# Kernel optimization log

Measured on AMD Instinct MI355X. Metric: run time of the kernel, lower is better.

The kernel has to match this reference:

```python
import jax, jax.numpy as jnp
import numpy as np

H = 32  # hidden size


def _lstm_layer(x_sbi, w_ih, w_hh, b_ih, b_hh):
    # x_sbi: [S, B, in]; w_ih: [4H, in]; w_hh: [4H, H] (torch gate order i,f,g,o)
    S, B, _ = x_sbi.shape
    # precompute input projections for all timesteps: [S, B, 4H]
    xg = jnp.einsum('sbi,gi->sbg', x_sbi, w_ih) + (b_ih + b_hh)

    def step(carry, xg_t):
        h, c = carry
        gates = xg_t + h @ w_hh.T  # [B, 4H]
        i, f, g, o = jnp.split(gates, 4, axis=-1)
        i = jax.nn.sigmoid(i)
        f = jax.nn.sigmoid(f)
        g = jnp.tanh(g)
        o = jax.nn.sigmoid(o)
        c = f * c + i * g
        h = o * jnp.tanh(c)
        return (h, c), h

    h0 = jnp.zeros((B, H), x_sbi.dtype)
    c0 = jnp.zeros((B, H), x_sbi.dtype)
    (h_last, _), hs = jax.lax.scan(step, (h0, c0), xg)
    return hs, h_last  # hs: [S, B, H]


def setup_inputs() -> dict:
    key = jax.random.key(0)
    ks = jax.random.split(key, 12)
    B, S = 4096, 512
    s = 1.0 / np.sqrt(H)  # torch default uniform(-1/sqrt(H), 1/sqrt(H))
    u = lambda k, shape: jax.random.uniform(k, shape, jnp.float32, -s, s)
    return {
        'x': jax.random.normal(ks[0], (B, S, 1), jnp.float32),
        'w_ih0': u(ks[1], (4 * H, 1)),
        'w_hh0': u(ks[2], (4 * H, H)),
        'b_ih0': u(ks[3], (4 * H,)),
        'b_hh0': u(ks[4], (4 * H,)),
        'w_ih1': u(ks[5], (4 * H, H)),
        'w_hh1': u(ks[6], (4 * H, H)),
        'b_ih1': u(ks[7], (4 * H,)),
        'b_hh1': u(ks[8], (4 * H,)),
        'fc1_w': u(ks[9], (16, H)),
        'fc1_b': u(ks[9], (16,)),
        'fc2_w': u(ks[10], (1, 16)),
        'fc2_b': u(ks[11], (1,)),
    }


def reference(x, w_ih0, w_hh0, b_ih0, b_hh0, w_ih1, w_hh1, b_ih1, b_hh1,
              fc1_w, fc1_b, fc2_w, fc2_b):
    x_sbi = jnp.swapaxes(x, 0, 1)  # [S, B, 1]
    hs1, _ = _lstm_layer(x_sbi, w_ih0, w_hh0, b_ih0, b_hh0)
    _, h_last = _lstm_layer(hs1, w_ih1, w_hh1, b_ih1, b_hh1)  # last timestep of layer 2
    y = h_last @ fc1_w.T + fc1_b
    y = jnp.where(y >= 0, y, 0.2 * y)  # leaky_relu(0.2)
    y = y @ fc2_w.T + fc2_b
    return y  # [B, 1]
```

## Files before the change

kernel.cpp:

```cpp
#include <hip/hip_runtime.h>

#define H 32
#define SEQ 512
#define BM 16
#define NTHREADS 512
#define HSTRIDE 40

typedef _Float16 half8 __attribute__((ext_vector_type(8)));
typedef __attribute__((ext_vector_type(4))) float f32x4;

#define L2E 1.44269504088896340736f

__device__ __forceinline__ float rcp_(float x)  { return __builtin_amdgcn_rcpf(x); }
__device__ __forceinline__ float exp2_(float x) { return __builtin_amdgcn_exp2f(x); }
#define MFMA16(A, B, C) __builtin_amdgcn_mfma_f32_16x16x32_f16((A), (B), (C), 0, 0, 0)

__device__ __forceinline__ float cell(const f32x4& g, float& cst) {
    float ei = exp2_(g[0]), ef = exp2_(g[1]), eg = exp2_(g[2]), eo = exp2_(g[3]);
    float A  = 1.f + ei, F = 1.f + ef;
    float Gp = eg + 1.f, Gm = eg - 1.f;
    float t1 = A * Gp;
    float num = fmaf(cst, t1, Gm * F);
    float cn  = num * rcp_(F * t1);
    cst = cn;
    float ec = exp2_(fminf(cn * (2.f * L2E), 80.f));
    return (ec - 1.f) * rcp_((1.f + eo) * (ec + 1.f));
}

__global__ __launch_bounds__(NTHREADS, 2) void lstm_kernel(
    const float* __restrict__ x,
    const float* __restrict__ w_ih0,
    const float* __restrict__ w_hh0,
    const float* __restrict__ b_ih0, const float* __restrict__ b_hh0,
    const float* __restrict__ w_ih1,
    const float* __restrict__ w_hh1,
    const float* __restrict__ b_ih1, const float* __restrict__ b_hh1,
    const float* __restrict__ fc1_w,
    const float* __restrict__ fc1_b,
    const float* __restrict__ fc2_w,
    const float* __restrict__ fc2_b,
    float* __restrict__ out)
{
    __shared__ __align__(16) float    xbufT[SEQ * BM];
    __shared__ __align__(16) _Float16 h1s[4][BM * HSTRIDE];
    __shared__ __align__(16) _Float16 h2s[2][BM * HSTRIDE];
    __shared__ __align__(16) float    h2f[BM * 33];
    __shared__ __align__(16) float    yb[BM * 17];

    const int tid  = threadIdx.x;
    const int lane = tid & 63;
    const int wv   = tid >> 6;
    const int role = wv >> 2;
    const int w    = wv & 3;
    const int c    = lane & 15;
    const int q    = lane >> 4;
    const int r0   = blockIdx.x * BM;

    {
        const int row = tid >> 5;
        const int s0  = (tid & 31) * 16;
        const float* xr = x + (size_t)(r0 + row) * SEQ + s0;
        #pragma unroll
        for (int i = 0; i < 16; i += 4) {
            float4 v = *(const float4*)&xr[i];
            xbufT[(s0 + i + 0) * BM + row] = v.x;
            xbufT[(s0 + i + 1) * BM + row] = v.y;
            xbufT[(s0 + i + 2) * BM + row] = v.z;
            xbufT[(s0 + i + 3) * BM + row] = v.w;
        }
    }
    for (int i = tid; i < 4 * BM * HSTRIDE; i += NTHREADS) ((_Float16*)h1s)[i] = (_Float16)0.f;
    for (int i = tid; i < 2 * BM * HSTRIDE; i += NTHREADS) ((_Float16*)h2s)[i] = (_Float16)0.f;

    const float gsc[4] = { -L2E, -L2E, 2.f * L2E, -L2E };
    const float wsc = gsc[c & 3];
    const int kb = 8 * q;
    const int m = c;

    half8 wA[2], wB[2];
    f32x4 biasv[2], wxv[2];
    int   wof[2];
    #pragma unroll
    for (int k = 0; k < 2; ++k) {
        const int u0    = 8 * w + 4 * k;
        const int u     = u0 + q;
        const int worig = (c & 3) * H + u0 + (c >> 2);
        wof[k] = m * HSTRIDE + u;
        if (role == 0) {
            const float* p = &w_hh0[worig * H + kb];
            #pragma unroll
            for (int j = 0; j < 8; ++j) wA[k][j] = (_Float16)(p[j] * wsc);
            #pragma unroll
            for (int g = 0; g < 4; ++g) {
                biasv[k][g] = (b_ih0[g * H + u] + b_hh0[g * H + u]) * gsc[g];
                wxv[k][g]   = w_ih0[g * H + u] * gsc[g];
            }
        } else {
            const float* p = &w_ih1[worig * H + kb];
            #pragma unroll
            for (int j = 0; j < 8; ++j) wA[k][j] = (_Float16)(p[j] * wsc);
            p = &w_hh1[worig * H + kb];
            #pragma unroll
            for (int j = 0; j < 8; ++j) wB[k][j] = (_Float16)(p[j] * wsc);
            #pragma unroll
            for (int g = 0; g < 4; ++g)
                biasv[k][g] = (b_ih1[g * H + u] + b_hh1[g * H + u]) * gsc[g];
        }
    }

    float cst[2] = {0.f, 0.f};
    float hl[2]  = {0.f, 0.f};

    const int fofs = c * HSTRIDE + kb;

    __syncthreads();

    if (role == 0) __builtin_amdgcn_s_setprio(1);

    float xv = xbufT[m];

    for (int tb = 0; tb < 516; tb += 4) {
        #pragma unroll
        for (int p = 0; p < 4; ++p) {
            const int t = tb + p;
            if (role == 0) {
                if (t < 512) {
                    f32x4 pre[2];
                    #pragma unroll
                    for (int k = 0; k < 2; ++k) {
                        #pragma unroll
                        for (int j = 0; j < 4; ++j) pre[k][j] = fmaf(xv, wxv[k][j], biasv[k][j]);
                    }
                    half8 a1 = *(const half8*)(&h1s[(p + 3) & 3][0] + fofs);
                    f32x4 g1[2];
                    #pragma unroll
                    for (int k = 0; k < 2; ++k) g1[k] = MFMA16(wA[k], a1, pre[k]);
                    #pragma unroll
                    for (int k = 0; k < 2; ++k) {
                        float hv = cell(g1[k], cst[k]);
                        h1s[p][wof[k]] = (_Float16)hv;
                    }
                    int tn = t + 1 < 511 ? t + 1 : 511;
                    xv = xbufT[tn * BM + m];
                }
            } else {
                if (t >= 2 && t < 514) {
                    half8 a1L = *(const half8*)(&h1s[(p + 2) & 3][0] + fofs);
                    half8 a2  = *(const half8*)(&h2s[(p + 1) & 1][0] + fofs);
                    f32x4 g2[2];
                    #pragma unroll
                    for (int k = 0; k < 2; ++k) g2[k] = MFMA16(wB[k], a2, MFMA16(wA[k], a1L, biasv[k]));
                    #pragma unroll
                    for (int k = 0; k < 2; ++k) {
                        float hv = cell(g2[k], cst[k]);
                        hl[k] = hv;
                        h2s[p & 1][wof[k]] = (_Float16)hv;
                    }
                }
            }
            __syncthreads();
        }
    }

    if (role == 0) __builtin_amdgcn_s_setprio(0);

    if (role == 1) {
        #pragma unroll
        for (int k = 0; k < 2; ++k) h2f[m * 33 + (8 * w + 4 * k + q)] = hl[k];
    }
    __syncthreads();
    if (tid < BM * 16) {
        int rr = tid >> 4, j = tid & 15;
        float acc = fc1_b[j];
        #pragma unroll
        for (int k = 0; k < H; ++k) acc += fc1_w[j * H + k] * h2f[rr * 33 + k];
        acc = acc >= 0.f ? acc : 0.2f * acc;
        yb[rr * 17 + j] = acc * fc2_w[j];
    }
    __syncthreads();
    if (tid < BM) {
        float acc = fc2_b[0];
        #pragma unroll
        for (int j = 0; j < 16; ++j) acc += yb[tid * 17 + j];
        out[r0 + tid] = acc;
    }
}

extern "C" void kernel_launch(void* const* d_in, const int* in_sizes, int n_in,
                              void* d_out, int out_size, void* d_ws, size_t ws_size,
                              hipStream_t stream) {
    const float* x     = (const float*)d_in[0];
    const float* w_ih0 = (const float*)d_in[1];
    const float* w_hh0 = (const float*)d_in[2];
    const float* b_ih0 = (const float*)d_in[3];
    const float* b_hh0 = (const float*)d_in[4];
    const float* w_ih1 = (const float*)d_in[5];
    const float* w_hh1 = (const float*)d_in[6];
    const float* b_ih1 = (const float*)d_in[7];
    const float* b_hh1 = (const float*)d_in[8];
    const float* fc1_w = (const float*)d_in[9];
    const float* fc1_b = (const float*)d_in[10];
    const float* fc2_w = (const float*)d_in[11];
    const float* fc2_b = (const float*)d_in[12];
    float* out = (float*)d_out;

    const int B = in_sizes[0] / SEQ;
    hipLaunchKernelGGL(lstm_kernel, dim3(B / BM), dim3(NTHREADS), 0, stream,
                       x, w_ih0, w_hh0, b_ih0, b_hh0, w_ih1, w_hh1, b_ih1, b_hh1,
                       fc1_w, fc1_b, fc2_w, fc2_b, out);
}
```

Before: 264.1 us.

## Precompute layer-2 input projection one step ahead and pack cell math as pairs

Layer-2 waves now compute the W_ih1·h1 MFMA for the next timestep right after their current step, so only the W_hh1 MFMA sits on the recurrent critical path. Hidden-unit assignment is remapped so each lane owns two adjacent units. This allows packed f32x2 cell math and a single 32-bit f16x2 store to LDS. The x buffer gains one padding row so the clamp on the next-x index can be dropped. The cost is extra registers for the double-buffered partial gates, which could hurt occupancy at the 2-blocks launch bound.

```diff
diff --git a/kernel.cpp b/kernel.cpp
--- a/kernel.cpp
+++ b/kernel.cpp
@@ -7,7 +7,9 @@
 #define HSTRIDE 40
 
 typedef _Float16 half8 __attribute__((ext_vector_type(8)));
+typedef _Float16 f16x2 __attribute__((ext_vector_type(2)));
 typedef __attribute__((ext_vector_type(4))) float f32x4;
+typedef __attribute__((ext_vector_type(2))) float f32x2;
 
 #define L2E 1.44269504088896340736f
 
@@ -15,16 +17,24 @@
 __device__ __forceinline__ float exp2_(float x) { return __builtin_amdgcn_exp2f(x); }
 #define MFMA16(A, B, C) __builtin_amdgcn_mfma_f32_16x16x32_f16((A), (B), (C), 0, 0, 0)
 
-__device__ __forceinline__ float cell(const f32x4& g, float& cst) {
-    float ei = exp2_(g[0]), ef = exp2_(g[1]), eg = exp2_(g[2]), eo = exp2_(g[3]);
-    float A  = 1.f + ei, F = 1.f + ef;
-    float Gp = eg + 1.f, Gm = eg - 1.f;
-    float t1 = A * Gp;
-    float num = fmaf(cst, t1, Gm * F);
-    float cn  = num * rcp_(F * t1);
+__device__ __forceinline__ f32x2 cell2(const f32x4& ga, const f32x4& gb, f32x2& cst) {
+    f32x2 ei = {exp2_(ga[0]), exp2_(gb[0])};
+    f32x2 ef = {exp2_(ga[1]), exp2_(gb[1])};
+    f32x2 eg = {exp2_(ga[2]), exp2_(gb[2])};
+    f32x2 eo = {exp2_(ga[3]), exp2_(gb[3])};
+    f32x2 A  = 1.f + ei, F = 1.f + ef;
+    f32x2 Gp = eg + 1.f, Gm = eg - 1.f;
+    f32x2 t1 = A * Gp;
+    f32x2 num = __builtin_elementwise_fma(cst, t1, Gm * F);
+    f32x2 den = F * t1;
+    f32x2 r1 = {rcp_(den.x), rcp_(den.y)};
+    f32x2 cn = num * r1;
     cst = cn;
-    float ec = exp2_(fminf(cn * (2.f * L2E), 80.f));
-    return (ec - 1.f) * rcp_((1.f + eo) * (ec + 1.f));
+    f32x2 arg = __builtin_elementwise_min(cn * (2.f * L2E), (f32x2)80.f);
+    f32x2 ec = {exp2_(arg.x), exp2_(arg.y)};
+    f32x2 dh = (1.f + eo) * (ec + 1.f);
+    f32x2 r2 = {rcp_(dh.x), rcp_(dh.y)};
+    return (ec - 1.f) * r2;
 }
 
 __global__ __launch_bounds__(NTHREADS, 2) void lstm_kernel(
@@ -41,7 +51,7 @@
     const float* __restrict__ fc2_b,
     float* __restrict__ out)
 {
-    __shared__ __align__(16) float    xbufT[SEQ * BM];
+    __shared__ __align__(16) float    xbufT[(SEQ + 1) * BM];
     __shared__ __align__(16) _Float16 h1s[4][BM * HSTRIDE];
     __shared__ __align__(16) _Float16 h2s[2][BM * HSTRIDE];
     __shared__ __align__(16) float    h2f[BM * 33];
@@ -79,13 +89,10 @@
 
     half8 wA[2], wB[2];
     f32x4 biasv[2], wxv[2];
-    int   wof[2];
     #pragma unroll
     for (int k = 0; k < 2; ++k) {
-        const int u0    = 8 * w + 4 * k;
-        const int u     = u0 + q;
-        const int worig = (c & 3) * H + u0 + (c >> 2);
-        wof[k] = m * HSTRIDE + u;
+        const int u     = 8 * w + 2 * q + k;
+        const int worig = (c & 3) * H + 8 * w + 2 * (c >> 2) + k;
         if (role == 0) {
             const float* p = &w_hh0[worig * H + kb];
             #pragma unroll
@@ -108,10 +115,13 @@
         }
     }
 
-    float cst[2] = {0.f, 0.f};
-    float hl[2]  = {0.f, 0.f};
-
-    const int fofs = c * HSTRIDE + kb;
+    f32x2 cst = {0.f, 0.f};
+    f32x2 hl  = {0.f, 0.f};
+
+    const int fofs  = c * HSTRIDE + kb;
+    const int whofs = m * HSTRIDE + 8 * w + 2 * q;
+
+    f32x4 P[2][2] = {};
 
     __syncthreads();
 
@@ -132,30 +142,27 @@
                         for (int j = 0; j < 4; ++j) pre[k][j] = fmaf(xv, wxv[k][j], biasv[k][j]);
                     }
                     half8 a1 = *(const half8*)(&h1s[(p + 3) & 3][0] + fofs);
-                    f32x4 g1[2];
-                    #pragma unroll
-                    for (int k = 0; k < 2; ++k) g1[k] = MFMA16(wA[k], a1, pre[k]);
-                    #pragma unroll
-                    for (int k = 0; k < 2; ++k) {
-                        float hv = cell(g1[k], cst[k]);
-                        h1s[p][wof[k]] = (_Float16)hv;
-                    }
-                    int tn = t + 1 < 511 ? t + 1 : 511;
-                    xv = xbufT[tn * BM + m];
+                    f32x4 g0 = MFMA16(wA[0], a1, pre[0]);
+                    f32x4 g1 = MFMA16(wA[1], a1, pre[1]);
+                    f32x2 hv = cell2(g0, g1, cst);
+                    f16x2 hp; hp[0] = (_Float16)hv.x; hp[1] = (_Float16)hv.y;
+                    *(f16x2*)(&h1s[p][0] + whofs) = hp;
+                    xv = xbufT[(t + 1) * BM + m];
                 }
             } else {
                 if (t >= 2 && t < 514) {
-                    half8 a1L = *(const half8*)(&h1s[(p + 2) & 3][0] + fofs);
-                    half8 a2  = *(const half8*)(&h2s[(p + 1) & 1][0] + fofs);
-                    f32x4 g2[2];
-                    #pragma unroll
-                    for (int k = 0; k < 2; ++k) g2[k] = MFMA16(wB[k], a2, MFMA16(wA[k], a1L, biasv[k]));
-                    #pragma unroll
-                    for (int k = 0; k < 2; ++k) {
-                        float hv = cell(g2[k], cst[k]);
-                        hl[k] = hv;
-                        h2s[p & 1][wof[k]] = (_Float16)hv;
-                    }
+                    half8 a2 = *(const half8*)(&h2s[(p + 1) & 1][0] + fofs);
+                    f32x4 g0 = MFMA16(wB[0], a2, P[p & 1][0]);
+                    f32x4 g1 = MFMA16(wB[1], a2, P[p & 1][1]);
+                    f32x2 hv = cell2(g0, g1, cst);
+                    hl = hv;
+                    f16x2 hp; hp[0] = (_Float16)hv.x; hp[1] = (_Float16)hv.y;
+                    *(f16x2*)(&h2s[p & 1][0] + whofs) = hp;
+                }
+                if (t >= 1 && t < 513) {
+                    half8 a1n = *(const half8*)(&h1s[(p + 3) & 3][0] + fofs);
+                    P[(p + 1) & 1][0] = MFMA16(wA[0], a1n, biasv[0]);
+                    P[(p + 1) & 1][1] = MFMA16(wA[1], a1n, biasv[1]);
                 }
             }
             __syncthreads();
@@ -165,8 +172,8 @@
     if (role == 0) __builtin_amdgcn_s_setprio(0);
 
     if (role == 1) {
-        #pragma unroll
-        for (int k = 0; k < 2; ++k) h2f[m * 33 + (8 * w + 4 * k + q)] = hl[k];
+        h2f[m * 33 + (8 * w + 2 * q + 0)] = hl.x;
+        h2f[m * 33 + (8 * w + 2 * q + 1)] = hl.y;
     }
     __syncthreads();
     if (tid < BM * 16) {
```

Result: faster. 253.6 us, median of 3 (-4.0%).

## Halve batch tile to 8 rows, split cell work across MFMA columns, prefetch layer-2 input projection

Applied to the files above, without the earlier changes.

Reduces the rows per block from 16 to 8 and doubles the blocks per CU, so twice as many blocks run the sequential recurrence in parallel. The 16 MFMA columns now hold 8 batch rows twice, and each lane evaluates a single LSTM cell by picking one of the two MFMA outputs, which halves the transcendental work per lane. Layer 2 computes its input-projection MFMA one step ahead into a double-buffered accumulator, taking it off the critical path. The cost is half the MFMA columns doing duplicated work and a doubled block count.

```diff
diff --git a/kernel.cpp b/kernel.cpp
--- a/kernel.cpp
+++ b/kernel.cpp
@@ -2,7 +2,7 @@
 
 #define H 32
 #define SEQ 512
-#define BM 16
+#define BM 8
 #define NTHREADS 512
 #define HSTRIDE 40
 
@@ -27,7 +27,7 @@
     return (ec - 1.f) * rcp_((1.f + eo) * (ec + 1.f));
 }
 
-__global__ __launch_bounds__(NTHREADS, 2) void lstm_kernel(
+__global__ __launch_bounds__(NTHREADS, 4) void lstm_kernel(
     const float* __restrict__ x,
     const float* __restrict__ w_ih0,
     const float* __restrict__ w_hh0,
@@ -41,7 +41,7 @@
     const float* __restrict__ fc2_b,
     float* __restrict__ out)
 {
-    __shared__ __align__(16) float    xbufT[SEQ * BM];
+    __shared__ __align__(16) float    xbufT[(SEQ + 1) * BM];
     __shared__ __align__(16) _Float16 h1s[4][BM * HSTRIDE];
     __shared__ __align__(16) _Float16 h2s[2][BM * HSTRIDE];
     __shared__ __align__(16) float    h2f[BM * 33];
@@ -54,19 +54,21 @@
     const int w    = wv & 3;
     const int c    = lane & 15;
     const int q    = lane >> 4;
+    const int row  = c & 7;
+    const int ch   = c >> 3;
     const int r0   = blockIdx.x * BM;
 
     {
-        const int row = tid >> 5;
-        const int s0  = (tid & 31) * 16;
-        const float* xr = x + (size_t)(r0 + row) * SEQ + s0;
-        #pragma unroll
-        for (int i = 0; i < 16; i += 4) {
+        const int xrow = tid >> 6;
+        const int s0   = (tid & 63) * 8;
+        const float* xr = x + (size_t)(r0 + xrow) * SEQ + s0;
+        #pragma unroll
+        for (int i = 0; i < 8; i += 4) {
             float4 v = *(const float4*)&xr[i];
-            xbufT[(s0 + i + 0) * BM + row] = v.x;
-            xbufT[(s0 + i + 1) * BM + row] = v.y;
-            xbufT[(s0 + i + 2) * BM + row] = v.z;
-            xbufT[(s0 + i + 3) * BM + row] = v.w;
+            xbufT[(s0 + i + 0) * BM + xrow] = v.x;
+            xbufT[(s0 + i + 1) * BM + xrow] = v.y;
+            xbufT[(s0 + i + 2) * BM + xrow] = v.z;
+            xbufT[(s0 + i + 3) * BM + xrow] = v.w;
         }
     }
     for (int i = tid; i < 4 * BM * HSTRIDE; i += NTHREADS) ((_Float16*)h1s)[i] = (_Float16)0.f;
@@ -75,17 +77,13 @@
     const float gsc[4] = { -L2E, -L2E, 2.f * L2E, -L2E };
     const float wsc = gsc[c & 3];
     const int kb = 8 * q;
-    const int m = c;
 
     half8 wA[2], wB[2];
     f32x4 biasv[2], wxv[2];
-    int   wof[2];
     #pragma unroll
     for (int k = 0; k < 2; ++k) {
-        const int u0    = 8 * w + 4 * k;
-        const int u     = u0 + q;
-        const int worig = (c & 3) * H + u0 + (c >> 2);
-        wof[k] = m * HSTRIDE + u;
+        const int u     = 8 * w + 2 * q + k;
+        const int worig = (c & 3) * H + 8 * w + 2 * (c >> 2) + k;
         if (role == 0) {
             const float* p = &w_hh0[worig * H + kb];
             #pragma unroll
@@ -108,16 +106,19 @@
         }
     }
 
-    float cst[2] = {0.f, 0.f};
-    float hl[2]  = {0.f, 0.f};
-
-    const int fofs = c * HSTRIDE + kb;
+    float cst = 0.f;
+    float hl  = 0.f;
+
+    const int fofs  = row * HSTRIDE + kb;
+    const int whofs = row * HSTRIDE + 8 * w + 2 * q + ch;
+
+    f32x4 P[2][2] = {};
 
     __syncthreads();
 
     if (role == 0) __builtin_amdgcn_s_setprio(1);
 
-    float xv = xbufT[m];
+    float xv = xbufT[row];
 
     for (int tb = 0; tb < 516; tb += 4) {
         #pragma unroll
@@ -125,37 +126,38 @@
             const int t = tb + p;
             if (role == 0) {
                 if (t < 512) {
-                    f32x4 pre[2];
+                    f32x4 pre0, pre1;
                     #pragma unroll
-                    for (int k = 0; k < 2; ++k) {
-                        #pragma unroll
-                        for (int j = 0; j < 4; ++j) pre[k][j] = fmaf(xv, wxv[k][j], biasv[k][j]);
+                    for (int j = 0; j < 4; ++j) {
+                        pre0[j] = fmaf(xv, wxv[0][j], biasv[0][j]);
+                        pre1[j] = fmaf(xv, wxv[1][j], biasv[1][j]);
                     }
                     half8 a1 = *(const half8*)(&h1s[(p + 3) & 3][0] + fofs);
-                    f32x4 g1[2];
+                    f32x4 g0 = MFMA16(wA[0], a1, pre0);
+                    f32x4 g1 = MFMA16(wA[1], a1, pre1);
+                    f32x4 g;
                     #pragma unroll
-                    for (int k = 0; k < 2; ++k) g1[k] = MFMA16(wA[k], a1, pre[k]);
-                    #pragma unroll
-                    for (int k = 0; k < 2; ++k) {
-                        float hv = cell(g1[k], cst[k]);
-                        h1s[p][wof[k]] = (_Float16)hv;
-                    }
-                    int tn = t + 1 < 511 ? t + 1 : 511;
-                    xv = xbufT[tn * BM + m];
+                    for (int j = 0; j < 4; ++j) g[j] = ch ? g1[j] : g0[j];
+                    float hv = cell(g, cst);
+                    h1s[p][whofs] = (_Float16)hv;
+                    xv = xbufT[(t + 1) * BM + row];
                 }
             } else {
                 if (t >= 2 && t < 514) {
-                    half8 a1L = *(const half8*)(&h1s[(p + 2) & 3][0] + fofs);
-                    half8 a2  = *(const half8*)(&h2s[(p + 1) & 1][0] + fofs);
-                    f32x4 g2[2];
+                    half8 a2 = *(const half8*)(&h2s[(p + 1) & 1][0] + fofs);
+                    f32x4 g0 = MFMA16(wB[0], a2, P[p & 1][0]);
+                    f32x4 g1 = MFMA16(wB[1], a2, P[p & 1][1]);
+                    f32x4 g;
                     #pragma unroll
-                    for (int k = 0; k < 2; ++k) g2[k] = MFMA16(wB[k], a2, MFMA16(wA[k], a1L, biasv[k]));
-                    #pragma unroll
-                    for (int k = 0; k < 2; ++k) {
-                        float hv = cell(g2[k], cst[k]);
-                        hl[k] = hv;
-                        h2s[p & 1][wof[k]] = (_Float16)hv;
-                    }
+                    for (int j = 0; j < 4; ++j) g[j] = ch ? g1[j] : g0[j];
+                    float hv = cell(g, cst);
+                    hl = hv;
+                    h2s[p & 1][whofs] = (_Float16)hv;
+                }
+                if (t >= 1 && t < 513) {
+                    half8 a1n = *(const half8*)(&h1s[(p + 3) & 3][0] + fofs);
+                    P[(p + 1) & 1][0] = MFMA16(wA[0], a1n, biasv[0]);
+                    P[(p + 1) & 1][1] = MFMA16(wA[1], a1n, biasv[1]);
                 }
             }
             __syncthreads();
@@ -164,10 +166,7 @@
 
     if (role == 0) __builtin_amdgcn_s_setprio(0);
 
-    if (role == 1) {
-        #pragma unroll
-        for (int k = 0; k < 2; ++k) h2f[m * 33 + (8 * w + 4 * k + q)] = hl[k];
-    }
+    if (role == 1) h2f[row * 33 + (8 * w + 2 * q + ch)] = hl;
     __syncthreads();
     if (tid < BM * 16) {
         int rr = tid >> 4, j = tid & 15;
```

Result: slower. 301.1 us (+14.0%).
